# Performance work log

Hardware: AMD Instinct MI355X
Metric: run time of the kernel (lower is better)

Reference implementation:

```python
import jax, jax.numpy as jnp
import numpy as np

N_HEADS = 16
ATT_DIM = 1024
HEAD_DIM = ATT_DIM // N_HEADS
SCALE = 1.0 / (HEAD_DIM ** 0.5)


def setup_inputs() -> dict:
    key = jax.random.key(0)
    k1, k2 = jax.random.split(key)
    B, N, D = 4, 2048, 1024
    X = jax.random.normal(k1, (B, N, D), dtype=jnp.float32)
    W_qkv = jax.random.normal(k2, (3 * ATT_DIM, D), dtype=jnp.float32) * 0.02  # trunc_normal-ish std
    return {"X": X, "W_qkv": W_qkv}


def reference(X, W_qkv):
    B, N, D = X.shape
    # qkv projection (bias=False): X @ W^T -> [b, n, 3*att_dim]
    QKV = jnp.einsum('bnd,od->bno', X, W_qkv)
    # rearrange 'b n (p h d) -> p b h n d'
    QKV = QKV.reshape(B, N, 3, N_HEADS, HEAD_DIM).transpose(2, 0, 3, 1, 4)
    Q, K, V = QKV[0], QKV[1], QKV[2]
    # scaled dot-product attention, full NxN scores (as in source)
    scores = jnp.einsum('bhid,bhjd->bhij', Q, K) * SCALE
    S = jax.nn.softmax(scores, axis=-1)
    # dropout rate is 0.0 -> identity
    Y = jnp.einsum('bhij,bhjd->bhid', S, V)
    # 'b h n d -> b n (h d)'; out_proj is Identity (out_dim == att_dim)
    return Y.transpose(0, 2, 1, 3).reshape(B, N, N_HEADS * HEAD_DIM)
```

## Files before the change

kernel.cpp:

```cpp
#include <hip/hip_runtime.h>

#define BATCH   4
#define SEQ     2048
#define DMODEL  1024
#define NHEADS  16
#define HDIM    64
#define QSC     0.18033688f

typedef short s16x8 __attribute__((ext_vector_type(8)));
typedef float f32x4 __attribute__((ext_vector_type(4)));
typedef const __attribute__((address_space(1))) unsigned int* gas_t;
typedef __attribute__((address_space(3))) unsigned int* las_t;

__device__ inline unsigned short f2bf(float f) {
    unsigned int u = __float_as_uint(f);
    u += 0x7FFF + ((u >> 16) & 1);
    return (unsigned short)(u >> 16);
}

__device__ __forceinline__ float exp2_fast(float x) {
#if __has_builtin(__builtin_amdgcn_exp2f)
    return __builtin_amdgcn_exp2f(x);
#else
    return exp2f(x);
#endif
}

__device__ __forceinline__ float rcp_fast(float x) {
#if __has_builtin(__builtin_amdgcn_rcpf)
    return __builtin_amdgcn_rcpf(x);
#else
    return 1.0f / x;
#endif
}

__device__ __forceinline__ unsigned int pack_bf16x2(float lo, float hi) {
    unsigned int a = __float_as_uint(lo) + 0x8000u;
    unsigned int b = __float_as_uint(hi) + 0x8000u;
#if __has_builtin(__builtin_amdgcn_perm)
    return __builtin_amdgcn_perm(b, a, 0x07060302u);
#else
    return (a >> 16) | (b & 0xFFFF0000u);
#endif
}

__global__ void cvt_bf16(const float* __restrict__ in,
                         unsigned short* __restrict__ out, int n4) {
    int i = blockIdx.x * blockDim.x + threadIdx.x;
    if (i >= n4) return;
    float4 v = ((const float4*)in)[i];
    ushort4 o;
    o.x = f2bf(v.x); o.y = f2bf(v.y); o.z = f2bf(v.z); o.w = f2bf(v.w);
    ((ushort4*)out)[i] = o;
}

__global__ __launch_bounds__(256) void qkv_gemm(
    const unsigned short* __restrict__ Xb,
    const unsigned short* __restrict__ Wb,
    unsigned short* __restrict__ Qo,
    unsigned short* __restrict__ Ko,
    unsigned short* __restrict__ Vt)
{
    __shared__ __align__(16) unsigned short As[128 * 32];
    __shared__ __align__(16) unsigned short Bs[128 * 32];

    const int t    = threadIdx.x;
    const int flat = blockIdx.y * 24 + blockIdx.x;
    const int sw   = (flat & 7) * 192 + (flat >> 3);
    const int m0   = (sw / 24) * 128;
    const int n0   = (sw % 24) * 128;

    const int wid  = t >> 6;
    const int lane = t & 63;
    const int l15  = lane & 15;
    const int quad = lane >> 4;
    const int wm   = (wid >> 1) * 64;
    const int wn   = (wid & 1) * 64;

    const int rA   = wid * 32 + (lane >> 2);
    const int kcol = (lane & 3) * 8;
    const unsigned short* gA = &Xb[(size_t)(m0 + rA) * 1024 + kcol];
    const unsigned short* gB = &Wb[(size_t)(n0 + rA) * 1024 + kcol];

    f32x4 acc[4][4] = {};

    for (int k0 = 0; k0 < 1024; k0 += 32) {
        __syncthreads();
        #pragma unroll
        for (int rd = 0; rd < 2; rd++) {
            __builtin_amdgcn_global_load_lds(
                (gas_t)(const void*)(gA + rd * 16 * 1024 + k0),
                (las_t)(void*)&As[(rA + rd * 16) * 32 + kcol], 16, 0, 0);
            __builtin_amdgcn_global_load_lds(
                (gas_t)(const void*)(gB + rd * 16 * 1024 + k0),
                (las_t)(void*)&Bs[(rA + rd * 16) * 32 + kcol], 16, 0, 0);
        }
        __syncthreads();

        s16x8 af[4], bf[4];
        #pragma unroll
        for (int mt = 0; mt < 4; mt++)
            af[mt] = *(const s16x8*)&As[(wm + mt * 16 + l15) * 32 + quad * 8];
        #pragma unroll
        for (int nt = 0; nt < 4; nt++)
            bf[nt] = *(const s16x8*)&Bs[(wn + nt * 16 + l15) * 32 + quad * 8];
        #pragma unroll
        for (int mt = 0; mt < 4; mt++)
            #pragma unroll
            for (int nt = 0; nt < 4; nt++)
                acc[mt][nt] = __builtin_amdgcn_mfma_f32_16x16x32_bf16(
                    af[mt], bf[nt], acc[mt][nt], 0, 0, 0);
    }

    #pragma unroll
    for (int mt = 0; mt < 4; mt++) {
        const int mbase = m0 + wm + mt * 16 + quad * 4;
        const int b     = mbase >> 11;
        const int nbase = mbase & 2047;
        #pragma unroll
        for (int nt = 0; nt < 4; nt++) {
            const int o  = n0 + wn + nt * 16 + l15;
            const int p  = o >> 10;
            const int oo = o & 1023;
            const int h  = oo >> 6;
            const int d  = oo & 63;
            if (p == 0) {
                #pragma unroll
                for (int r = 0; r < 4; r++)
                    Qo[((size_t)(b * 16 + h) * 2048 + nbase + r) * 64 + d] =
                        f2bf(acc[mt][nt][r] * QSC);
            } else if (p == 1) {
                #pragma unroll
                for (int r = 0; r < 4; r++)
                    Ko[((size_t)(b * 16 + h) * 2048 + nbase + r) * 64 + d] =
                        f2bf(acc[mt][nt][r]);
            } else {
                ushort4 v4;
                v4.x = f2bf(acc[mt][nt][0]);
                v4.y = f2bf(acc[mt][nt][1]);
                v4.z = f2bf(acc[mt][nt][2]);
                v4.w = f2bf(acc[mt][nt][3]);
                *(ushort4*)&Vt[((size_t)(b * 16 + h) * 64 + d) * 2048 + nbase] = v4;
            }
        }
    }
}

#define PSTRIDE 72
#define PBASE   16384

__global__ __launch_bounds__(256) void attn(
    const unsigned short* __restrict__ Q,
    const unsigned short* __restrict__ K,
    const unsigned short* __restrict__ Vt,
    float* __restrict__ out)
{
    __shared__ __align__(16) unsigned short LDS[PBASE + 4 * 32 * PSTRIDE];

    const int t    = threadIdx.x;
    const int w    = t >> 6;
    const int lane = t & 63;
    const int l15  = lane & 15;
    const int quad = lane >> 4;
    const int flat = blockIdx.y * 16 + blockIdx.x;
    const int sw   = (flat & 7) * 128 + (flat >> 3);
    const int head = sw >> 4;
    const int b    = head >> 4;
    const int h    = head & 15;
    const int q0   = (sw & 15) * 128 + w * 32;

    const unsigned short* Qh = Q  + (size_t)head * 2048 * 64;
    const unsigned short* Kh = K  + (size_t)head * 2048 * 64;
    const unsigned short* Vh = Vt + (size_t)head * 64 * 2048;

    const int r0 = t >> 3;
    const int c0 = (t & 7) ^ (r0 & 7);
    const unsigned short* srcK = Kh + r0 * 64 + c0 * 8;
    const unsigned short* srcV = Vh + r0 * 2048 + c0 * 8;

    auto stageKV = [&](int kt, int bufE) {
        #pragma unroll
        for (int rd = 0; rd < 2; rd++) {
            __builtin_amdgcn_global_load_lds(
                (gas_t)(const void*)(srcK + kt * 4096 + rd * 2048),
                (las_t)(void*)&LDS[bufE + rd * 2048 + w * 512], 16, 0, 0);
            __builtin_amdgcn_global_load_lds(
                (gas_t)(const void*)(srcV + kt * 64 + rd * 65536),
                (las_t)(void*)&LDS[bufE + 4096 + rd * 2048 + w * 512], 16, 0, 0);
        }
    };

    s16x8 qb[2][2];
    #pragma unroll
    for (int mt = 0; mt < 2; mt++)
        #pragma unroll
        for (int kc = 0; kc < 2; kc++)
            qb[mt][kc] = *(const s16x8*)&Qh[(size_t)(q0 + mt * 16 + l15) * 64 + kc * 32 + quad * 8];

    f32x4 y[2][4] = {};
    float lsum[2] = {0.f, 0.f};
    unsigned short* P = &LDS[PBASE + w * (32 * PSTRIDE)];

    const int x7   = l15 & 7;
    const int csw0 = (quad ^ x7) * 8;
    const int csw1 = ((4 + quad) ^ x7) * 8;

    auto compute = [&](int bufE) {
        s16x8 kb[4][2];
        #pragma unroll
        for (int nt = 0; nt < 4; nt++) {
            const int rowb = bufE + (nt * 16 + l15) * 64;
            kb[nt][0] = *(const s16x8*)&LDS[rowb + csw0];
            kb[nt][1] = *(const s16x8*)&LDS[rowb + csw1];
        }
        f32x4 st[4][2] = {};
        #pragma unroll
        for (int kc = 0; kc < 2; kc++)
            #pragma unroll
            for (int nt = 0; nt < 4; nt++)
                #pragma unroll
                for (int mt = 0; mt < 2; mt++)
                    st[nt][mt] = __builtin_amdgcn_mfma_f32_16x16x32_bf16(
                        kb[nt][kc], qb[mt][kc], st[nt][mt], 0, 0, 0);
        s16x8 vb[4][2];
        #pragma unroll
        for (int dt = 0; dt < 4; dt++) {
            const int rowb = bufE + 4096 + (dt * 16 + l15) * 64;
            vb[dt][0] = *(const s16x8*)&LDS[rowb + csw0];
            vb[dt][1] = *(const s16x8*)&LDS[rowb + csw1];
        }
        #pragma unroll
        for (int mt = 0; mt < 2; mt++)
            #pragma unroll
            for (int nt = 0; nt < 4; nt++) {
                float p0 = exp2_fast(st[nt][mt][0]);
                float p1 = exp2_fast(st[nt][mt][1]);
                float p2 = exp2_fast(st[nt][mt][2]);
                float p3 = exp2_fast(st[nt][mt][3]);
                lsum[mt] += (p0 + p1) + (p2 + p3);
                uint2 u;
                u.x = pack_bf16x2(p0, p1);
                u.y = pack_bf16x2(p2, p3);
                *(uint2*)&P[(mt * 16 + l15) * PSTRIDE + nt * 16 + quad * 4] = u;
            }
        #pragma unroll
        for (int kc = 0; kc < 2; kc++) {
            s16x8 pa[2];
            #pragma unroll
            for (int mt = 0; mt < 2; mt++)
                pa[mt] = *(const s16x8*)&P[(mt * 16 + l15) * PSTRIDE + kc * 32 + quad * 8];
            #pragma unroll
            for (int mt = 0; mt < 2; mt++)
                #pragma unroll
                for (int dt = 0; dt < 4; dt++)
                    y[mt][dt] = __builtin_amdgcn_mfma_f32_16x16x32_bf16(
                        pa[mt], vb[dt][kc], y[mt][dt], 0, 0, 0);
        }
    };

    stageKV(0, 0);
    __syncthreads();

    #pragma unroll 1
    for (int kt = 0; kt < 32; kt += 2) {
        stageKV(kt + 1, 8192);
        compute(0);
        __syncthreads();
        if (kt + 2 < 32) stageKV(kt + 2, 0);
        compute(8192);
        __syncthreads();
    }

    #pragma unroll
    for (int mt = 0; mt < 2; mt++) {
        float v = lsum[mt];
        v += __shfl_xor(v, 16);
        v += __shfl_xor(v, 32);
        lsum[mt] = v;
    }

    float rinv[2][4];
    #pragma unroll
    for (int mt = 0; mt < 2; mt++)
        #pragma unroll
        for (int r = 0; r < 4; r++)
            rinv[mt][r] = rcp_fast(__shfl(lsum[mt], quad * 4 + r));

    #pragma unroll
    for (int mt = 0; mt < 2; mt++)
        #pragma unroll
        for (int dt = 0; dt < 4; dt++)
            #pragma unroll
            for (int r = 0; r < 4; r++) {
                const int n = q0 + mt * 16 + quad * 4 + r;
                const int d = dt * 16 + l15;
                out[((size_t)(b * 2048 + n)) * 1024 + h * 64 + d] =
                    y[mt][dt][r] * rinv[mt][r];
            }
}

extern "C" void kernel_launch(void* const* d_in, const int* in_sizes, int n_in,
                              void* d_out, int out_size, void* d_ws, size_t ws_size,
                              hipStream_t stream) {
    const float* X = (const float*)d_in[0];
    const float* W = (const float*)d_in[1];
    float* out = (float*)d_out;

    char* ws = (char*)d_ws;
    unsigned short* Xb = (unsigned short*)(ws);
    unsigned short* Wb = (unsigned short*)(ws + 16777216);
    unsigned short* Qb = (unsigned short*)(ws + 23068672);
    unsigned short* Kb = (unsigned short*)(ws + 39845888);
    unsigned short* Vt = (unsigned short*)(ws + 56623104);

    cvt_bf16<<<dim3(8192), dim3(256), 0, stream>>>(X, Xb, 2097152);
    cvt_bf16<<<dim3(3072), dim3(256), 0, stream>>>(W, Wb, 786432);
    qkv_gemm<<<dim3(24, 64), dim3(256), 0, stream>>>(Xb, Wb, Qb, Kb, Vt);
    attn<<<dim3(16, 64), dim3(256), 0, stream>>>(Qb, Kb, Vt, out);
}
```

Measured before the change: 255.4 us.

## Compute softmax row sums via MFMA with ones vector and simplify block mapping

Replaces the per-lane VALU accumulation of exponentials plus cross-lane shuffles with an extra MFMA that multiplies the bf16 P tile by a vector of ones, so row sums come out in the same layout as the output accumulator. It also splits the QK MFMA chain to start from a zero accumulator and removes the swizzled block-to-head mapping in favour of direct blockIdx indexing. The sum now uses bf16-rounded probabilities, which matches the values used in PV, and it adds MFMA work. Dropping the swizzle may change L2 locality for K/V reuse.

```diff
diff --git a/kernel.cpp b/kernel.cpp
--- a/kernel.cpp
+++ b/kernel.cpp
@@ -162,12 +162,10 @@
     const int lane = t & 63;
     const int l15  = lane & 15;
     const int quad = lane >> 4;
-    const int flat = blockIdx.y * 16 + blockIdx.x;
-    const int sw   = (flat & 7) * 128 + (flat >> 3);
-    const int head = sw >> 4;
+    const int head = blockIdx.y;
     const int b    = head >> 4;
     const int h    = head & 15;
-    const int q0   = (sw & 15) * 128 + w * 32;
+    const int q0   = blockIdx.x * 128 + w * 32;
 
     const unsigned short* Qh = Q  + (size_t)head * 2048 * 64;
     const unsigned short* Kh = K  + (size_t)head * 2048 * 64;
@@ -197,8 +195,13 @@
         for (int kc = 0; kc < 2; kc++)
             qb[mt][kc] = *(const s16x8*)&Qh[(size_t)(q0 + mt * 16 + l15) * 64 + kc * 32 + quad * 8];
 
+    s16x8 onesf;
+    #pragma unroll
+    for (int i = 0; i < 8; i++) onesf[i] = (short)0x3F80;
+    const f32x4 fz = {0.f, 0.f, 0.f, 0.f};
+
     f32x4 y[2][4] = {};
-    float lsum[2] = {0.f, 0.f};
+    f32x4 ysum[2] = {};
     unsigned short* P = &LDS[PBASE + w * (32 * PSTRIDE)];
 
     const int x7   = l15 & 7;
@@ -213,15 +216,19 @@
             kb[nt][0] = *(const s16x8*)&LDS[rowb + csw0];
             kb[nt][1] = *(const s16x8*)&LDS[rowb + csw1];
         }
-        f32x4 st[4][2] = {};
-        #pragma unroll
-        for (int kc = 0; kc < 2; kc++)
-            #pragma unroll
-            for (int nt = 0; nt < 4; nt++)
-                #pragma unroll
-                for (int mt = 0; mt < 2; mt++)
-                    st[nt][mt] = __builtin_amdgcn_mfma_f32_16x16x32_bf16(
-                        kb[nt][kc], qb[mt][kc], st[nt][mt], 0, 0, 0);
+        f32x4 st[4][2];
+        #pragma unroll
+        for (int nt = 0; nt < 4; nt++)
+            #pragma unroll
+            for (int mt = 0; mt < 2; mt++)
+                st[nt][mt] = __builtin_amdgcn_mfma_f32_16x16x32_bf16(
+                    kb[nt][0], qb[mt][0], fz, 0, 0, 0);
+        #pragma unroll
+        for (int nt = 0; nt < 4; nt++)
+            #pragma unroll
+            for (int mt = 0; mt < 2; mt++)
+                st[nt][mt] = __builtin_amdgcn_mfma_f32_16x16x32_bf16(
+                    kb[nt][1], qb[mt][1], st[nt][mt], 0, 0, 0);
         s16x8 vb[4][2];
         #pragma unroll
         for (int dt = 0; dt < 4; dt++) {
@@ -237,7 +244,6 @@
                 float p1 = exp2_fast(st[nt][mt][1]);
                 float p2 = exp2_fast(st[nt][mt][2]);
                 float p3 = exp2_fast(st[nt][mt][3]);
-                lsum[mt] += (p0 + p1) + (p2 + p3);
                 uint2 u;
                 u.x = pack_bf16x2(p0, p1);
                 u.y = pack_bf16x2(p2, p3);
@@ -249,6 +255,10 @@
             #pragma unroll
             for (int mt = 0; mt < 2; mt++)
                 pa[mt] = *(const s16x8*)&P[(mt * 16 + l15) * PSTRIDE + kc * 32 + quad * 8];
+            #pragma unroll
+            for (int mt = 0; mt < 2; mt++)
+                ysum[mt] = __builtin_amdgcn_mfma_f32_16x16x32_bf16(
+                    pa[mt], onesf, ysum[mt], 0, 0, 0);
             #pragma unroll
             for (int mt = 0; mt < 2; mt++)
                 #pragma unroll
@@ -271,20 +281,12 @@
         __syncthreads();
     }
 
-    #pragma unroll
-    for (int mt = 0; mt < 2; mt++) {
-        float v = lsum[mt];
-        v += __shfl_xor(v, 16);
-        v += __shfl_xor(v, 32);
-        lsum[mt] = v;
-    }
-
     float rinv[2][4];
     #pragma unroll
     for (int mt = 0; mt < 2; mt++)
         #pragma unroll
         for (int r = 0; r < 4; r++)
-            rinv[mt][r] = rcp_fast(__shfl(lsum[mt], quad * 4 + r));
+            rinv[mt][r] = rcp_fast(ysum[mt][r]);
 
     #pragma unroll
     for (int mt = 0; mt < 2; mt++)
```

Result: no change. 252.4 us (-1.2%).
